# Kernel optimization log

Measured on AMD Instinct MI355X. Metric: run time of the kernel, lower is better.

## Reference

```python
import jax, jax.numpy as jnp
import numpy as np

N = 50000      # nodes
E = 800000     # edges (before self-loops)
D = 128        # input_dim == hidden_dim
L = 3          # num_layers
EPS = 1e-5     # BatchNorm eps


def setup_inputs() -> dict:
    key = jax.random.key(0)
    k0, k1, k2 = jax.random.split(key, 3)
    x = jax.random.normal(k0, (N, D), dtype=jnp.float32)
    edge_index = jax.random.randint(k1, (2, E), 0, N, dtype=jnp.int32)
    # stacked per-layer params (layer 0 is input_dim->hidden, same shape since D==hidden)
    W = jax.random.normal(k2, (L, D, D), dtype=jnp.float32) / np.float32(np.sqrt(D))
    b = jnp.zeros((L, D), dtype=jnp.float32)
    gamma = jnp.ones((L, D), dtype=jnp.float32)
    beta = jnp.zeros((L, D), dtype=jnp.float32)
    return {"x": x, "edge_index": edge_index, "W": W, "b": b, "gamma": gamma, "beta": beta}


def reference(x, edge_index, W, b, gamma, beta):
    # --- GCN symmetric normalization with self-loops (PyG GCNConv default) ---
    loop = jnp.arange(N, dtype=edge_index.dtype)
    src = jnp.concatenate([edge_index[0], loop])      # [E+N]
    dst = jnp.concatenate([edge_index[1], loop])      # [E+N]
    deg = jax.ops.segment_sum(jnp.ones_like(dst, dtype=x.dtype), dst, num_segments=N)
    dinv = jax.lax.rsqrt(deg)                          # deg >= 1 due to self-loops
    norm = (dinv[src] * dinv[dst])[:, None]            # [E+N, 1]

    h = x
    for i in range(L):
        # GCNConv: aggregate norm * (h W)[src] into dst, then bias
        m = h @ W[i]                                   # [N, D]
        h = jax.ops.segment_sum(m[src] * norm, dst, num_segments=N) + b[i]
        # BatchNorm1d (training-mode batch statistics, biased variance)
        mu = jnp.mean(h, axis=0)
        var = jnp.var(h, axis=0)
        h = gamma[i] * (h - mu) * jax.lax.rsqrt(var + EPS) + beta[i]
        # ReLU; dropout is identity in eval mode
        h = jax.nn.relu(h)
    return h
```

## Files before the change

### kernel.cpp

```cpp
#include <hip/hip_runtime.h>
#include <hip/hip_bf16.h>

#define N_NODES 50000
#define N_EDGES 800000
#define DIM 128
#define BN_EPS 1e-5f
#define GATHER_BLOCKS (N_NODES / 4)
#define RED_BLOCKS 125
#define CAP 48

#define PART_SHIFT 7
#define PART_SIZE 128
#define NPARTS ((N_NODES + PART_SIZE - 1) / PART_SIZE)
#define QSTRIDE 32
#define BIN_EPB 4096
#define BIN_BLOCKS ((N_EDGES + BIN_EPB - 1) / BIN_EPB)
#define QCAP2 2560
#define GEMM_BLOCKS (N_NODES / 16)

typedef __attribute__((ext_vector_type(8))) short short8;
typedef __attribute__((ext_vector_type(4))) float float4v;

__device__ __forceinline__ float bf16_bits_to_f32(unsigned short u) {
    union { unsigned int i; float f; } c;
    c.i = ((unsigned int)u) << 16;
    return c.f;
}

__device__ __forceinline__ float bf16_lo(unsigned int u) {
    union { unsigned int i; float f; } c;
    c.i = u << 16;
    return c.f;
}

__device__ __forceinline__ float bf16_hi(unsigned int u) {
    union { unsigned int i; float f; } c;
    c.i = u & 0xFFFF0000u;
    return c.f;
}

__device__ __forceinline__ unsigned short f32_to_bf16_bits(float f) {
    union { float f; unsigned int i; } c;
    c.f = f;
    unsigned int lsb = (c.i >> 16) & 1u;
    c.i += 0x7FFFu + lsb;
    return (unsigned short)(c.i >> 16);
}

__global__ __launch_bounds__(256) void sniff(const unsigned short* __restrict__ xu,
                                             float* __restrict__ mode) {
    __shared__ int cnt;
    if (threadIdx.x == 0) cnt = 0;
    __syncthreads();
    int ok = 0;
    for (int i = threadIdx.x; i < 512; i += 256) {
        unsigned e = (xu[i] >> 7) & 0xFFu;
        if (e >= 96u && e <= 159u) ok++;
    }
    atomicAdd(&cnt, ok);
    __syncthreads();
    if (threadIdx.x == 0) mode[0] = (cnt >= 480) ? 0.0f : 1.0f;
}

__global__ __launch_bounds__(256) void zero_buf(float* __restrict__ p, int n) {
    int i = blockIdx.x * blockDim.x + threadIdx.x;
    if (i < n) p[i] = 0.0f;
}

__global__ __launch_bounds__(256) void zero_int(int* __restrict__ p, int n) {
    int i = blockIdx.x * blockDim.x + threadIdx.x;
    if (i < n) p[i] = 0;
}

__global__ __launch_bounds__(256) void zero_aux(int* __restrict__ qcnt,
                                                float* __restrict__ stats,
                                                int* __restrict__ done) {
    for (int i = threadIdx.x; i < NPARTS; i += 256) qcnt[(size_t)i * QSTRIDE] = 0;
    stats[threadIdx.x] = 0.0f;
    if (threadIdx.x == 0) done[0] = 0;
}

__global__ __launch_bounds__(256) void convert_params(
    const void* __restrict__ W, const void* __restrict__ b,
    const void* __restrict__ g, const void* __restrict__ be,
    const float* __restrict__ mode,
    unsigned short* __restrict__ Wt, float* __restrict__ pf32) {
    const bool mf32 = mode[0] > 0.5f;
    int i = blockIdx.x * blockDim.x + threadIdx.x;
    const int NW = 3 * DIM * DIM;
    if (i < NW) {
        int l = i >> 14;
        int rem = i & 16383;
        int k = rem >> 7;
        int n = rem & 127;
        unsigned short v = mf32 ? f32_to_bf16_bits(((const float*)W)[i])
                                : ((const unsigned short*)W)[i];
        Wt[(size_t)l * DIM * DIM + (size_t)n * DIM + k] = v;
    } else if (i < NW + 3 * 3 * DIM) {
        int p = i - NW;
        int which = p / 384;
        int r = p - which * 384;
        const void* srcp = (which == 0) ? b : (which == 1) ? g : be;
        float v = mf32 ? ((const float*)srcp)[r]
                       : bf16_bits_to_f32(((const unsigned short*)srcp)[r]);
        pf32[which * 384 + r] = v;
    }
}

__global__ __launch_bounds__(256) void fused_a(
    const int* __restrict__ src, const int* __restrict__ dst,
    int* __restrict__ qcnt, unsigned int* __restrict__ queue,
    const void* __restrict__ x, const unsigned short* __restrict__ Wt,
    const float* __restrict__ mode, unsigned short* __restrict__ A) {
    __shared__ int lcnt[NPARTS];
    __shared__ int pref[NPARTS];
    __shared__ int loff[NPARTS];
    __shared__ int gbase[NPARTS];
    __shared__ unsigned int staged2[BIN_EPB];
    __shared__ int sortedN;
    const int bid = blockIdx.x;
    if (bid < BIN_BLOCKS) {
        const int t = threadIdx.x;
        const int blk0 = bid * BIN_EPB;
        const int nval = min(BIN_EPB, N_EDGES - blk0);
        for (int i = t; i < NPARTS; i += 256) lcnt[i] = 0;
        __syncthreads();
        for (int li = t; li < nval; li += 256) {
            int d = dst[blk0 + li];
            if ((unsigned)d < (unsigned)N_NODES)
                atomicAdd(&lcnt[d >> PART_SHIFT], 1);
        }
        __syncthreads();
        if (t < 64) {
            int base = 0;
            for (int c = 0; c < (NPARTS + 63) / 64; ++c) {
                int idx = c * 64 + t;
                int orig = (idx < NPARTS) ? lcnt[idx] : 0;
                int v = orig;
                #pragma unroll
                for (int o = 1; o < 64; o <<= 1) {
                    int up = __shfl_up(v, o);
                    if (t >= o) v += up;
                }
                if (idx < NPARTS) { pref[idx] = base + v - orig; loff[idx] = base + v - orig; }
                base += __shfl(v, 63);
            }
            if (t == 0) sortedN = base;
        }
        __syncthreads();
        for (int i = t; i < NPARTS; i += 256) {
            int c = lcnt[i];
            gbase[i] = c ? atomicAdd(&qcnt[(size_t)i * QSTRIDE], c) : 0;
        }
        __syncthreads();
        for (int li = t; li < nval; li += 256) {
            int d = dst[blk0 + li];
            if ((unsigned)d < (unsigned)N_NODES) {
                int s = src[blk0 + li];
                int part = d >> PART_SHIFT;
                unsigned int pk = (unsigned int)(s & 0xFFFF) |
                                  ((unsigned int)(d & (PART_SIZE - 1)) << 16) |
                                  ((unsigned int)part << 23);
                int pos = atomicAdd(&loff[part], 1);
                staged2[pos] = pk;
            }
        }
        __syncthreads();
        const int nOut = sortedN;
        for (int i = t; i < nOut; i += 256) {
            unsigned int pk = staged2[i];
            int part = pk >> 23;
            int gp = gbase[part] + (i - pref[part]);
            if (gp < QCAP2)
                queue[(size_t)part * QCAP2 + gp] = pk;
        }
        return;
    }
    const int wave = threadIdx.x >> 6;
    const int lane = threadIdx.x & 63;
    const int quad = lane >> 4;
    const int nidx = lane & 15;
    const int row0 = (bid - BIN_BLOCKS) * 16;

    short8 afrag[4];
    if (mode[0] > 0.5f) {
        const float* xf = (const float*)x;
        #pragma unroll
        for (int kk = 0; kk < 4; ++kk) {
            const float4v* xr = (const float4v*)(xf + (size_t)(row0 + nidx) * DIM + kk * 32 + quad * 8);
            float4v p0 = xr[0], p1 = xr[1];
            #pragma unroll
            for (int j = 0; j < 4; ++j) {
                afrag[kk][j]     = (short)f32_to_bf16_bits(p0[j]);
                afrag[kk][4 + j] = (short)f32_to_bf16_bits(p1[j]);
            }
        }
    } else {
        const unsigned short* hu = (const unsigned short*)x;
        #pragma unroll
        for (int kk = 0; kk < 4; ++kk)
            afrag[kk] = *(const short8*)(hu + (size_t)(row0 + nidx) * DIM + kk * 32 + quad * 8);
    }

    short8 bfrag[2][4];
    #pragma unroll
    for (int half = 0; half < 2; ++half) {
        int c = wave * 32 + half * 16 + nidx;
        #pragma unroll
        for (int kk = 0; kk < 4; ++kk)
            bfrag[half][kk] = *(const short8*)(Wt + (size_t)c * DIM + kk * 32 + quad * 8);
    }

    float4v acc0 = {0.f, 0.f, 0.f, 0.f};
    float4v acc1 = {0.f, 0.f, 0.f, 0.f};
    #pragma unroll
    for (int kk = 0; kk < 4; ++kk) {
        acc0 = __builtin_amdgcn_mfma_f32_16x16x32_bf16(afrag[kk], bfrag[0][kk], acc0, 0, 0, 0);
        acc1 = __builtin_amdgcn_mfma_f32_16x16x32_bf16(afrag[kk], bfrag[1][kk], acc1, 0, 0, 0);
    }

    #pragma unroll
    for (int r = 0; r < 4; ++r) {
        int row = row0 + quad * 4 + r;
        size_t i0 = (size_t)row * DIM + wave * 32 + nidx;
        A[i0]      = f32_to_bf16_bits(acc0[r]);
        A[i0 + 16] = f32_to_bf16_bits(acc1[r]);
    }
}

__global__ __launch_bounds__(256) void csr_build(
    const int* __restrict__ qcnt, const unsigned int* __restrict__ queue,
    unsigned short* __restrict__ colu, int* __restrict__ cnt,
    float* __restrict__ dinv) {
    __shared__ int lcnt[PART_SIZE];
    const int p = blockIdx.x;
    if (threadIdx.x < PART_SIZE) lcnt[threadIdx.x] = 0;
    __syncthreads();
    const int base = p << PART_SHIFT;
    const int n = min(qcnt[(size_t)p * QSTRIDE], QCAP2);
    const unsigned int* qp = queue + (size_t)p * QCAP2;
    for (int i = threadIdx.x; i < n; i += 256) {
        unsigned int pk = qp[i];
        int dl = (pk >> 16) & (PART_SIZE - 1);
        int s  = pk & 0xFFFFu;
        int pos = atomicAdd(&lcnt[dl], 1);
        if (pos < CAP)
            colu[(size_t)(base + dl) * CAP + pos] = (unsigned short)s;
    }
    __syncthreads();
    if (threadIdx.x < PART_SIZE) {
        int d = base + threadIdx.x;
        if (d < N_NODES) {
            int c = lcnt[threadIdx.x];
            cnt[d] = c;
            dinv[d] = rsqrtf((float)c + 1.0f);
        }
    }
}

__global__ __launch_bounds__(256) void make_dinv(const int* __restrict__ cnt,
                                                 float* __restrict__ dinv) {
    int v = blockIdx.x * blockDim.x + threadIdx.x;
    if (v < N_NODES) dinv[v] = rsqrtf((float)cnt[v] + 1.0f);
}

__global__ __launch_bounds__(256) void gemm_scale(
    const void* hsrc, int kind, int b_bf16,
    const unsigned short* __restrict__ Wt,
    const float* __restrict__ dinv,
    const float* __restrict__ mode,
    const float* __restrict__ alpha, const float* __restrict__ delta,
    unsigned short* A, float* __restrict__ B, int write_b) {
    const int wave = threadIdx.x >> 6;
    const int lane = threadIdx.x & 63;
    const int quad = lane >> 4;
    const int nidx = lane & 15;
    const int row0 = blockIdx.x * 16;

    short8 afrag[4];
    if (kind == 0) {
        if (mode[0] > 0.5f) {
            const float* xf = (const float*)hsrc;
            #pragma unroll
            for (int kk = 0; kk < 4; ++kk) {
                const float4v* xr = (const float4v*)(xf + (size_t)(row0 + nidx) * DIM + kk * 32 + quad * 8);
                float4v p0 = xr[0], p1 = xr[1];
                #pragma unroll
                for (int j = 0; j < 4; ++j) {
                    afrag[kk][j]     = (short)f32_to_bf16_bits(p0[j]);
                    afrag[kk][4 + j] = (short)f32_to_bf16_bits(p1[j]);
                }
            }
        } else {
            const unsigned short* hu = (const unsigned short*)hsrc;
            #pragma unroll
            for (int kk = 0; kk < 4; ++kk)
                afrag[kk] = *(const short8*)(hu + (size_t)(row0 + nidx) * DIM + kk * 32 + quad * 8);
        }
    } else if (b_bf16) {
        const unsigned short* Bh = (const unsigned short*)hsrc;
        const float dv = dinv[row0 + nidx];
        #pragma unroll
        for (int kk = 0; kk < 4; ++kk) {
            short8 braw = *(const short8*)(Bh + (size_t)(row0 + nidx) * DIM + kk * 32 + quad * 8);
            const float* ap = alpha + kk * 32 + quad * 8;
            const float* dp = delta + kk * 32 + quad * 8;
            float4v A0 = *(const float4v*)ap, A1 = *(const float4v*)(ap + 4);
            float4v D0 = *(const float4v*)dp, D1 = *(const float4v*)(dp + 4);
            #pragma unroll
            for (int j = 0; j < 4; ++j) {
                float v0 = bf16_bits_to_f32((unsigned short)braw[j]);
                float v1 = bf16_bits_to_f32((unsigned short)braw[4 + j]);
                float h0 = fmaxf(fmaf(A0[j] * dv, v0, D0[j]), 0.f);
                float h1 = fmaxf(fmaf(A1[j] * dv, v1, D1[j]), 0.f);
                afrag[kk][j]     = (short)f32_to_bf16_bits(h0);
                afrag[kk][4 + j] = (short)f32_to_bf16_bits(h1);
            }
        }
    } else {
        const float* Bf = (const float*)hsrc;
        const float dv = dinv[row0 + nidx];
        #pragma unroll
        for (int kk = 0; kk < 4; ++kk) {
            const float* bp = Bf + (size_t)(row0 + nidx) * DIM + kk * 32 + quad * 8;
            float4v p0 = *(const float4v*)bp;
            float4v p1 = *(const float4v*)(bp + 4);
            const float* ap = alpha + kk * 32 + quad * 8;
            const float* dp = delta + kk * 32 + quad * 8;
            float4v A0 = *(const float4v*)ap, A1 = *(const float4v*)(ap + 4);
            float4v D0 = *(const float4v*)dp, D1 = *(const float4v*)(dp + 4);
            #pragma unroll
            for (int j = 0; j < 4; ++j) {
                float h0 = fmaxf(fmaf(A0[j] * dv, p0[j], D0[j]), 0.f);
                float h1 = fmaxf(fmaf(A1[j] * dv, p1[j], D1[j]), 0.f);
                afrag[kk][j]     = (short)f32_to_bf16_bits(h0);
                afrag[kk][4 + j] = (short)f32_to_bf16_bits(h1);
            }
        }
    }

    short8 bfrag[2][4];
    #pragma unroll
    for (int half = 0; half < 2; ++half) {
        int c = wave * 32 + half * 16 + nidx;
        #pragma unroll
        for (int kk = 0; kk < 4; ++kk)
            bfrag[half][kk] = *(const short8*)(Wt + (size_t)c * DIM + kk * 32 + quad * 8);
    }

    float4v acc0 = {0.f, 0.f, 0.f, 0.f};
    float4v acc1 = {0.f, 0.f, 0.f, 0.f};
    #pragma unroll
    for (int kk = 0; kk < 4; ++kk) {
        acc0 = __builtin_amdgcn_mfma_f32_16x16x32_bf16(afrag[kk], bfrag[0][kk], acc0, 0, 0, 0);
        acc1 = __builtin_amdgcn_mfma_f32_16x16x32_bf16(afrag[kk], bfrag[1][kk], acc1, 0, 0, 0);
    }

    #pragma unroll
    for (int r = 0; r < 4; ++r) {
        int row = row0 + quad * 4 + r;
        float d = dinv[row];
        float v0 = acc0[r] * d;
        float v1 = acc1[r] * d;
        size_t i0 = (size_t)row * DIM + wave * 32 + nidx;
        size_t i1 = i0 + 16;
        A[i0] = f32_to_bf16_bits(v0);
        A[i1] = f32_to_bf16_bits(v1);
        if (write_b) { B[i0] = v0; B[i1] = v1; }
    }
}

#define ACC4(v, w) do { \
    if (SC) { a0 = fmaf(w, bf16_lo(v.x), a0); a1 = fmaf(w, bf16_hi(v.x), a1); \
              a2 = fmaf(w, bf16_lo(v.y), a2); a3 = fmaf(w, bf16_hi(v.y), a3); } \
    else { a0 += bf16_lo(v.x); a1 += bf16_hi(v.x); \
           a2 += bf16_lo(v.y); a3 += bf16_hi(v.y); } } while (0)

template <int SC>
__global__ __launch_bounds__(256) void gather_csr(
    const int* __restrict__ cnt, const unsigned short* __restrict__ colu,
    const unsigned short* __restrict__ A,
    const float* __restrict__ dinv, const float* __restrict__ bias,
    unsigned short* __restrict__ Bh, float* __restrict__ partial) {
    __shared__ float sacc[4][128], sacc2[4][128];
    const int wave = threadIdx.x >> 6;
    const int lane = threadIdx.x & 63;
    const int half = lane >> 5;
    const int lid  = lane & 31;
    const int cbase = lid * 4;
    const int node = blockIdx.x * 4 + wave;
    const int lo = node * CAP;
    const int hi = lo + min(cnt[node], CAP);
    const float dv = dinv[node];

    float a0 = 0.f, a1 = 0.f, a2 = 0.f, a3 = 0.f;
    if (half == 0) {
        uint2 su = *(const uint2*)(A + (size_t)node * DIM + cbase);
        const float scl = SC ? dv : 1.0f;
        a0 = scl * bf16_lo(su.x); a1 = scl * bf16_hi(su.x);
        a2 = scl * bf16_lo(su.y); a3 = scl * bf16_hi(su.y);
    }

    int e = lo + half;
    for (; e + 14 < hi; e += 16) {
        int s0 = colu[e];      int s1 = colu[e + 2];
        int s2 = colu[e + 4];  int s3 = colu[e + 6];
        int s4 = colu[e + 8];  int s5 = colu[e + 10];
        int s6 = colu[e + 12]; int s7 = colu[e + 14];
        float w0 = SC ? dinv[s0] : 0.f; float w1 = SC ? dinv[s1] : 0.f;
        float w2 = SC ? dinv[s2] : 0.f; float w3 = SC ? dinv[s3] : 0.f;
        float w4 = SC ? dinv[s4] : 0.f; float w5 = SC ? dinv[s5] : 0.f;
        float w6 = SC ? dinv[s6] : 0.f; float w7 = SC ? dinv[s7] : 0.f;
        uint2 v0 = *(const uint2*)(A + (size_t)s0 * DIM + cbase);
        uint2 v1 = *(const uint2*)(A + (size_t)s1 * DIM + cbase);
        uint2 v2 = *(const uint2*)(A + (size_t)s2 * DIM + cbase);
        uint2 v3 = *(const uint2*)(A + (size_t)s3 * DIM + cbase);
        uint2 v4 = *(const uint2*)(A + (size_t)s4 * DIM + cbase);
        uint2 v5 = *(const uint2*)(A + (size_t)s5 * DIM + cbase);
        uint2 v6 = *(const uint2*)(A + (size_t)s6 * DIM + cbase);
        uint2 v7 = *(const uint2*)(A + (size_t)s7 * DIM + cbase);
        ACC4(v0, w0); ACC4(v1, w1); ACC4(v2, w2); ACC4(v3, w3);
        ACC4(v4, w4); ACC4(v5, w5); ACC4(v6, w6); ACC4(v7, w7);
    }
    for (; e + 6 < hi; e += 8) {
        int s0 = colu[e];     int s1 = colu[e + 2];
        int s2 = colu[e + 4]; int s3 = colu[e + 6];
        float w0 = SC ? dinv[s0] : 0.f; float w1 = SC ? dinv[s1] : 0.f;
        float w2 = SC ? dinv[s2] : 0.f; float w3 = SC ? dinv[s3] : 0.f;
        uint2 v0 = *(const uint2*)(A + (size_t)s0 * DIM + cbase);
        uint2 v1 = *(const uint2*)(A + (size_t)s1 * DIM + cbase);
        uint2 v2 = *(const uint2*)(A + (size_t)s2 * DIM + cbase);
        uint2 v3 = *(const uint2*)(A + (size_t)s3 * DIM + cbase);
        ACC4(v0, w0); ACC4(v1, w1); ACC4(v2, w2); ACC4(v3, w3);
    }
    for (; e < hi; e += 2) {
        int s0 = colu[e];
        float w0 = SC ? dinv[s0] : 0.f;
        uint2 v0 = *(const uint2*)(A + (size_t)s0 * DIM + cbase);
        ACC4(v0, w0);
    }

    a0 += __shfl_xor(a0, 32);
    a1 += __shfl_xor(a1, 32);
    a2 += __shfl_xor(a2, 32);
    a3 += __shfl_xor(a3, 32);

    if (half == 0) {
        unsigned int px = (unsigned int)f32_to_bf16_bits(a0) |
                          ((unsigned int)f32_to_bf16_bits(a1) << 16);
        unsigned int py = (unsigned int)f32_to_bf16_bits(a2) |
                          ((unsigned int)f32_to_bf16_bits(a3) << 16);
        uint2 st = {px, py};
        *(uint2*)(Bh + (size_t)node * DIM + cbase) = st;
        float4 bb = *(const float4*)(bias + cbase);
        float v0 = fmaf(dv, a0, bb.x);
        float v1 = fmaf(dv, a1, bb.y);
        float v2 = fmaf(dv, a2, bb.z);
        float v3 = fmaf(dv, a3, bb.w);
        sacc[wave][cbase]     = v0;  sacc2[wave][cbase]     = v0 * v0;
        sacc[wave][cbase + 1] = v1;  sacc2[wave][cbase + 1] = v1 * v1;
        sacc[wave][cbase + 2] = v2;  sacc2[wave][cbase + 2] = v2 * v2;
        sacc[wave][cbase + 3] = v3;  sacc2[wave][cbase + 3] = v3 * v3;
    }
    __syncthreads();
    const int t = threadIdx.x;
    float s;
    if (t < 128) s = sacc[0][t] + sacc[1][t] + sacc[2][t] + sacc[3][t];
    else { int c = t - 128; s = sacc2[0][c] + sacc2[1][c] + sacc2[2][c] + sacc2[3][c]; }
    partial[(size_t)blockIdx.x * 256 + t] = s;
}

__global__ __launch_bounds__(256) void reduce_coefs(
    const float* __restrict__ partial, float* __restrict__ stats,
    int* __restrict__ done, const float* __restrict__ pf32, int l,
    float* __restrict__ alpha, float* __restrict__ delta) {
    const int t = threadIdx.x;
    const int rows = GATHER_BLOCKS / RED_BLOCKS;
    const int r0 = blockIdx.x * rows;
    float s = 0.f;
    for (int i = 0; i < rows; ++i)
        s += partial[(size_t)(r0 + i) * 256 + t];
    atomicAdd(&stats[t], s);
    __threadfence();
    __shared__ int lastFlag;
    if (t == 0) lastFlag = (atomicAdd(done, 1) == RED_BLOCKS - 1) ? 1 : 0;
    __syncthreads();
    if (lastFlag && t < 128) {
        float cs  = atomicAdd(&stats[t], 0.0f);
        float css = atomicAdd(&stats[t + 128], 0.0f);
        const float invN = 1.0f / N_NODES;
        float mu = cs * invN;
        float var = css * invN - mu * mu;
        float istd = rsqrtf(var + BN_EPS);
        float gg = pf32[384 + l * 128 + t];
        float bt = pf32[768 + l * 128 + t];
        float bi = pf32[l * 128 + t];
        float al = gg * istd;
        alpha[t] = al;
        delta[t] = al * (bi - mu) + bt;
        atomicExch(&stats[t], 0.0f);
        atomicExch(&stats[t + 128], 0.0f);
        if (t == 0) atomicExch(done, 0);
    }
}

__global__ __launch_bounds__(128) void bn_coefs(
    const float* __restrict__ pf32, int l,
    float* __restrict__ colsum, float* __restrict__ colsumsq,
    float* __restrict__ alpha, float* __restrict__ delta) {
    int c = threadIdx.x;
    const float invN = 1.0f / N_NODES;
    float mu = colsum[c] * invN;
    float var = colsumsq[c] * invN - mu * mu;
    float istd = rsqrtf(var + BN_EPS);
    float gg = pf32[384 + l * 128 + c];
    float bt = pf32[768 + l * 128 + c];
    float bi = pf32[l * 128 + c];
    float al = gg * istd;
    alpha[c] = al;
    delta[c] = al * (bi - mu) + bt;
    colsum[c] = 0.f;
    colsumsq[c] = 0.f;
}

__global__ __launch_bounds__(256) void hist_dst(const int* __restrict__ dst,
                                                int* __restrict__ cnt) {
    int e = blockIdx.x * blockDim.x + threadIdx.x;
    if (e < N_EDGES) atomicAdd(&cnt[dst[e]], 1);
}

__global__ __launch_bounds__(256) void scatter_edges(
    const int* __restrict__ src, const int* __restrict__ dst,
    const unsigned short* __restrict__ A, float* __restrict__ B) {
    int t = blockIdx.x * blockDim.x + threadIdx.x;
    int e = t >> 4;
    if (e >= N_EDGES) return;
    int f = (t & 15) * 8;
    int s = src[e], d = dst[e];
    short8 v = *(const short8*)(A + (size_t)s * DIM + f);
    float* bp = B + (size_t)d * DIM + f;
    #pragma unroll
    for (int j = 0; j < 8; ++j)
        atomicAdd(bp + j, bf16_bits_to_f32((unsigned short)v[j]));
}

__global__ __launch_bounds__(256) void bn_reduce(
    const float* __restrict__ B, const float* __restrict__ dinv,
    const float* __restrict__ bias,
    float* __restrict__ colsum, float* __restrict__ colsumsq) {
    int c = threadIdx.x & 127;
    int half = threadIdx.x >> 7;
    float bb = bias[c];
    float s = 0.f, s2 = 0.f;
    for (int row = blockIdx.x * 2 + half; row < N_NODES; row += gridDim.x * 2) {
        float v = dinv[row] * B[(size_t)row * DIM + c] + bb;
        s += v;
        s2 += v * v;
    }
    __shared__ float ls[128], ls2[128];
    if (half == 1) { ls[c] = s; ls2[c] = s2; }
    __syncthreads();
    if (half == 0) {
        atomicAdd(&colsum[c], s + ls[c]);
        atomicAdd(&colsumsq[c], s2 + ls2[c]);
    }
}

__global__ __launch_bounds__(256) void bn_apply(
    const void* __restrict__ Bv, int b_bf16,
    const float* __restrict__ dinv,
    const float* __restrict__ alpha, const float* __restrict__ delta,
    const float* __restrict__ mode, void* __restrict__ out) {
    int t = blockIdx.x * blockDim.x + threadIdx.x;
    if (t >= N_NODES * DIM) return;
    int row = t >> 7, c = t & 127;
    float bval = b_bf16 ? bf16_bits_to_f32(((const unsigned short*)Bv)[t])
                        : ((const float*)Bv)[t];
    float r = fmaxf(fmaf(alpha[c] * dinv[row], bval, delta[c]), 0.f);
    if (mode[0] > 0.5f)
        ((float*)out)[t] = r;
    else
        ((unsigned short*)out)[t] = f32_to_bf16_bits(r);
}

extern "C" void kernel_launch(void* const* d_in, const int* in_sizes, int n_in,
                              void* d_out, int out_size, void* d_ws, size_t ws_size,
                              hipStream_t stream) {
    const void* x  = d_in[0];
    const int*  ei = (const int*)d_in[1];
    const void* W  = d_in[2];
    const void* b  = d_in[3];
    const void* g  = d_in[4];
    const void* be = d_in[5];

    unsigned short* hA = (unsigned short*)d_out;

    char* ws = (char*)d_ws;
    size_t off = 0;
    auto alloc = [&](size_t bytes) {
        char* p = ws + off;
        off = (off + bytes + 255) & ~(size_t)255;
        return p;
    };
    float* dinv     = (float*)alloc((size_t)N_NODES * 4);
    float* B        = (float*)alloc((size_t)N_NODES * DIM * 4);
    unsigned short* Wt = (unsigned short*)alloc((size_t)3 * DIM * DIM * 2);
    float* pf32     = (float*)alloc(3 * 3 * DIM * 4);
    float* stats    = (float*)alloc(256 * 4);
    float* alphaB   = (float*)alloc(128 * 4);
    float* deltaB   = (float*)alloc(128 * 4);
    float* mode     = (float*)alloc(64 * 4);
    int*   done     = (int*)alloc(64 * 4);
    int*   cnt      = (int*)alloc((size_t)N_NODES * 4);
    unsigned short* colu = (unsigned short*)alloc((size_t)N_NODES * CAP * 2);
    float* partial  = (float*)alloc((size_t)GATHER_BLOCKS * 256 * 4);
    int*   qcnt     = (int*)alloc((size_t)NPARTS * QSTRIDE * 4);
    unsigned int* queue = (unsigned int*)partial;
    const bool csr_ok = (ws_size >= off) || (ws_size == 0);
    float* colsum = stats;
    float* colsumsq = stats + 128;
    unsigned short* Bh = (unsigned short*)B;

    const int* srcv = ei;
    const int* dstv = ei + N_EDGES;

    sniff<<<1, 256, 0, stream>>>((const unsigned short*)x, mode);
    convert_params<<<(3 * DIM * DIM + 3 * 3 * DIM + 255) / 256, 256, 0, stream>>>(
        W, b, g, be, mode, Wt, pf32);

    if (csr_ok) {
        zero_aux<<<1, 256, 0, stream>>>(qcnt, stats, done);
        fused_a<<<BIN_BLOCKS + GEMM_BLOCKS, 256, 0, stream>>>(
            srcv, dstv, qcnt, queue, x, Wt, mode, hA);
        csr_build<<<NPARTS, 256, 0, stream>>>(qcnt, queue, colu, cnt, dinv);

        for (int l = 0; l < 3; ++l) {
            if (l > 0)
                gemm_scale<<<GEMM_BLOCKS, 256, 0, stream>>>(
                    (const void*)B, 2, 1, Wt + (size_t)l * DIM * DIM, dinv, mode,
                    alphaB, deltaB, hA, B, 0);
            if (l == 0)
                gather_csr<1><<<GATHER_BLOCKS, 256, 0, stream>>>(
                    cnt, colu, hA, dinv, pf32 + l * 128, Bh, partial);
            else
                gather_csr<0><<<GATHER_BLOCKS, 256, 0, stream>>>(
                    cnt, colu, hA, dinv, pf32 + l * 128, Bh, partial);
            reduce_coefs<<<RED_BLOCKS, 256, 0, stream>>>(
                partial, stats, done, pf32, l, alphaB, deltaB);
            if (l == 2)
                bn_apply<<<(N_NODES * DIM) / 256, 256, 0, stream>>>(
                    (const void*)B, 1, dinv, alphaB, deltaB, mode, d_out);
        }
    } else {
        zero_int<<<(N_NODES + 255) / 256, 256, 0, stream>>>(cnt, N_NODES);
        zero_buf<<<1, 256, 0, stream>>>(stats, 256);
        hist_dst<<<(N_EDGES + 255) / 256, 256, 0, stream>>>(dstv, cnt);
        make_dinv<<<(N_NODES + 255) / 256, 256, 0, stream>>>(cnt, dinv);

        for (int l = 0; l < 3; ++l) {
            const void* hin = (l == 0) ? x : (const void*)B;
            gemm_scale<<<GEMM_BLOCKS, 256, 0, stream>>>(
                hin, (l == 0) ? 0 : 2, 0, Wt + (size_t)l * DIM * DIM, dinv, mode,
                alphaB, deltaB, hA, B, 1);
            scatter_edges<<<(N_EDGES * 16) / 256, 256, 0, stream>>>(srcv, dstv, hA, B);
            bn_reduce<<<256, 256, 0, stream>>>(B, dinv, pf32 + l * 128, colsum, colsumsq);
            bn_coefs<<<1, 128, 0, stream>>>(pf32, l, colsum, colsumsq, alphaB, deltaB);
            if (l == 2)
                bn_apply<<<(N_NODES * DIM) / 256, 256, 0, stream>>>(
                    (const void*)B, 0, dinv, alphaB, deltaB, mode, d_out);
        }
    }
}
```

Measured before the change: 351.8 us.

## Stage edge indices as 16-bit in binning and widen gather to 16-byte loads

```diff
diff --git a/kernel.cpp b/kernel.cpp
--- a/kernel.cpp
+++ b/kernel.cpp
@@ -113,10 +113,9 @@
     const void* __restrict__ x, const unsigned short* __restrict__ Wt,
     const float* __restrict__ mode, unsigned short* __restrict__ A) {
     __shared__ int lcnt[NPARTS];
-    __shared__ int pref[NPARTS];
     __shared__ int loff[NPARTS];
-    __shared__ int gbase[NPARTS];
-    __shared__ unsigned int staged2[BIN_EPB];
+    __shared__ int adj[NPARTS];
+    __shared__ unsigned short staged16[BIN_EPB];
     __shared__ int sortedN;
     const int bid = blockIdx.x;
     if (bid < BIN_BLOCKS) {
@@ -142,7 +141,7 @@
                     int up = __shfl_up(v, o);
                     if (t >= o) v += up;
                 }
-                if (idx < NPARTS) { pref[idx] = base + v - orig; loff[idx] = base + v - orig; }
+                if (idx < NPARTS) loff[idx] = base + v - orig;
                 base += __shfl(v, 63);
             }
             if (t == 0) sortedN = base;
@@ -150,29 +149,30 @@
         __syncthreads();
         for (int i = t; i < NPARTS; i += 256) {
             int c = lcnt[i];
-            gbase[i] = c ? atomicAdd(&qcnt[(size_t)i * QSTRIDE], c) : 0;
+            int gb = c ? atomicAdd(&qcnt[(size_t)i * QSTRIDE], c) : 0;
+            adj[i] = gb - loff[i];
         }
         __syncthreads();
         for (int li = t; li < nval; li += 256) {
             int d = dst[blk0 + li];
             if ((unsigned)d < (unsigned)N_NODES) {
-                int s = src[blk0 + li];
                 int part = d >> PART_SHIFT;
-                unsigned int pk = (unsigned int)(s & 0xFFFF) |
-                                  ((unsigned int)(d & (PART_SIZE - 1)) << 16) |
-                                  ((unsigned int)part << 23);
                 int pos = atomicAdd(&loff[part], 1);
-                staged2[pos] = pk;
+                staged16[pos] = (unsigned short)li;
             }
         }
         __syncthreads();
         const int nOut = sortedN;
         for (int i = t; i < nOut; i += 256) {
-            unsigned int pk = staged2[i];
-            int part = pk >> 23;
-            int gp = gbase[part] + (i - pref[part]);
-            if (gp < QCAP2)
-                queue[(size_t)part * QCAP2 + gp] = pk;
+            int li = staged16[i];
+            int d = dst[blk0 + li];
+            int s = src[blk0 + li];
+            int part = d >> PART_SHIFT;
+            int gp = adj[part] + i;
+            if (gp >= 0 && gp < QCAP2)
+                queue[(size_t)part * QCAP2 + gp] =
+                    (unsigned int)(s & 0xFFFF) |
+                    ((unsigned int)(d & (PART_SIZE - 1)) << 16);
         }
         return;
     }
@@ -370,11 +370,11 @@
     }
 }
 
-#define ACC4(v, w) do { \
-    if (SC) { a0 = fmaf(w, bf16_lo(v.x), a0); a1 = fmaf(w, bf16_hi(v.x), a1); \
-              a2 = fmaf(w, bf16_lo(v.y), a2); a3 = fmaf(w, bf16_hi(v.y), a3); } \
-    else { a0 += bf16_lo(v.x); a1 += bf16_hi(v.x); \
-           a2 += bf16_lo(v.y); a3 += bf16_hi(v.y); } } while (0)
+#define FMA8(vv, ww) do { \
+    a0 = fmaf(ww, bf16_lo(vv.x), a0); a1 = fmaf(ww, bf16_hi(vv.x), a1); \
+    a2 = fmaf(ww, bf16_lo(vv.y), a2); a3 = fmaf(ww, bf16_hi(vv.y), a3); \
+    a4 = fmaf(ww, bf16_lo(vv.z), a4); a5 = fmaf(ww, bf16_hi(vv.z), a5); \
+    a6 = fmaf(ww, bf16_lo(vv.w), a6); a7 = fmaf(ww, bf16_hi(vv.w), a7); } while (0)
 
 template <int SC>
 __global__ __launch_bounds__(256) void gather_csr(
@@ -385,82 +385,68 @@
     __shared__ float sacc[4][128], sacc2[4][128];
     const int wave = threadIdx.x >> 6;
     const int lane = threadIdx.x & 63;
-    const int half = lane >> 5;
-    const int lid  = lane & 31;
-    const int cbase = lid * 4;
+    const int g    = lane >> 4;
+    const int c8   = (lane & 15) * 8;
     const int node = blockIdx.x * 4 + wave;
-    const int lo = node * CAP;
-    const int hi = lo + min(cnt[node], CAP);
+    const int deg  = min(cnt[node], CAP);
+    const int lo   = node * CAP;
     const float dv = dinv[node];
 
-    float a0 = 0.f, a1 = 0.f, a2 = 0.f, a3 = 0.f;
-    if (half == 0) {
-        uint2 su = *(const uint2*)(A + (size_t)node * DIM + cbase);
-        const float scl = SC ? dv : 1.0f;
-        a0 = scl * bf16_lo(su.x); a1 = scl * bf16_hi(su.x);
-        a2 = scl * bf16_lo(su.y); a3 = scl * bf16_hi(su.y);
-    }
-
-    int e = lo + half;
-    for (; e + 14 < hi; e += 16) {
-        int s0 = colu[e];      int s1 = colu[e + 2];
-        int s2 = colu[e + 4];  int s3 = colu[e + 6];
-        int s4 = colu[e + 8];  int s5 = colu[e + 10];
-        int s6 = colu[e + 12]; int s7 = colu[e + 14];
-        float w0 = SC ? dinv[s0] : 0.f; float w1 = SC ? dinv[s1] : 0.f;
-        float w2 = SC ? dinv[s2] : 0.f; float w3 = SC ? dinv[s3] : 0.f;
-        float w4 = SC ? dinv[s4] : 0.f; float w5 = SC ? dinv[s5] : 0.f;
-        float w6 = SC ? dinv[s6] : 0.f; float w7 = SC ? dinv[s7] : 0.f;
-        uint2 v0 = *(const uint2*)(A + (size_t)s0 * DIM + cbase);
-        uint2 v1 = *(const uint2*)(A + (size_t)s1 * DIM + cbase);
-        uint2 v2 = *(const uint2*)(A + (size_t)s2 * DIM + cbase);
-        uint2 v3 = *(const uint2*)(A + (size_t)s3 * DIM + cbase);
-        uint2 v4 = *(const uint2*)(A + (size_t)s4 * DIM + cbase);
-        uint2 v5 = *(const uint2*)(A + (size_t)s5 * DIM + cbase);
-        uint2 v6 = *(const uint2*)(A + (size_t)s6 * DIM + cbase);
-        uint2 v7 = *(const uint2*)(A + (size_t)s7 * DIM + cbase);
-        ACC4(v0, w0); ACC4(v1, w1); ACC4(v2, w2); ACC4(v3, w3);
-        ACC4(v4, w4); ACC4(v5, w5); ACC4(v6, w6); ACC4(v7, w7);
-    }
-    for (; e + 6 < hi; e += 8) {
-        int s0 = colu[e];     int s1 = colu[e + 2];
-        int s2 = colu[e + 4]; int s3 = colu[e + 6];
-        float w0 = SC ? dinv[s0] : 0.f; float w1 = SC ? dinv[s1] : 0.f;
-        float w2 = SC ? dinv[s2] : 0.f; float w3 = SC ? dinv[s3] : 0.f;
-        uint2 v0 = *(const uint2*)(A + (size_t)s0 * DIM + cbase);
-        uint2 v1 = *(const uint2*)(A + (size_t)s1 * DIM + cbase);
-        uint2 v2 = *(const uint2*)(A + (size_t)s2 * DIM + cbase);
-        uint2 v3 = *(const uint2*)(A + (size_t)s3 * DIM + cbase);
-        ACC4(v0, w0); ACC4(v1, w1); ACC4(v2, w2); ACC4(v3, w3);
-    }
-    for (; e < hi; e += 2) {
-        int s0 = colu[e];
-        float w0 = SC ? dinv[s0] : 0.f;
-        uint2 v0 = *(const uint2*)(A + (size_t)s0 * DIM + cbase);
-        ACC4(v0, w0);
-    }
-
-    a0 += __shfl_xor(a0, 32);
-    a1 += __shfl_xor(a1, 32);
-    a2 += __shfl_xor(a2, 32);
-    a3 += __shfl_xor(a3, 32);
-
-    if (half == 0) {
-        unsigned int px = (unsigned int)f32_to_bf16_bits(a0) |
-                          ((unsigned int)f32_to_bf16_bits(a1) << 16);
-        unsigned int py = (unsigned int)f32_to_bf16_bits(a2) |
-                          ((unsigned int)f32_to_bf16_bits(a3) << 16);
-        uint2 st = {px, py};
-        *(uint2*)(Bh + (size_t)node * DIM + cbase) = st;
-        float4 bb = *(const float4*)(bias + cbase);
-        float v0 = fmaf(dv, a0, bb.x);
-        float v1 = fmaf(dv, a1, bb.y);
-        float v2 = fmaf(dv, a2, bb.z);
-        float v3 = fmaf(dv, a3, bb.w);
-        sacc[wave][cbase]     = v0;  sacc2[wave][cbase]     = v0 * v0;
-        sacc[wave][cbase + 1] = v1;  sacc2[wave][cbase + 1] = v1 * v1;
-        sacc[wave][cbase + 2] = v2;  sacc2[wave][cbase + 2] = v2 * v2;
-        sacc[wave][cbase + 3] = v3;  sacc2[wave][cbase + 3] = v3 * v3;
+    int   cv = (lane < deg) ? (int)colu[lo + lane] : 0;
+    float wv = (lane < deg) ? (SC ? dinv[cv] : 1.0f) : 0.0f;
+
+    float a0, a1, a2, a3, a4, a5, a6, a7;
+    {
+        uint4 sv = *(const uint4*)(A + (size_t)node * DIM + c8);
+        const float scl = (g == 0) ? (SC ? dv : 1.0f) : 0.0f;
+        a0 = scl * bf16_lo(sv.x); a1 = scl * bf16_hi(sv.x);
+        a2 = scl * bf16_lo(sv.y); a3 = scl * bf16_hi(sv.y);
+        a4 = scl * bf16_lo(sv.z); a5 = scl * bf16_hi(sv.z);
+        a6 = scl * bf16_lo(sv.w); a7 = scl * bf16_hi(sv.w);
+    }
+
+    const int rounds = (deg + 7) >> 3;
+    int j = 0;
+    for (int r = 0; r < rounds; ++r, j += 8) {
+        int   iA = j + g,  iB = j + 4 + g;
+        int   sA = __shfl(cv, iA);  float wA = __shfl(wv, iA);
+        int   sB = __shfl(cv, iB);  float wB = __shfl(wv, iB);
+        uint4 vA = *(const uint4*)(A + (size_t)sA * DIM + c8);
+        uint4 vB = *(const uint4*)(A + (size_t)sB * DIM + c8);
+        FMA8(vA, wA);
+        FMA8(vB, wB);
+    }
+
+    a0 += __shfl_xor(a0, 16); a0 += __shfl_xor(a0, 32);
+    a1 += __shfl_xor(a1, 16); a1 += __shfl_xor(a1, 32);
+    a2 += __shfl_xor(a2, 16); a2 += __shfl_xor(a2, 32);
+    a3 += __shfl_xor(a3, 16); a3 += __shfl_xor(a3, 32);
+    a4 += __shfl_xor(a4, 16); a4 += __shfl_xor(a4, 32);
+    a5 += __shfl_xor(a5, 16); a5 += __shfl_xor(a5, 32);
+    a6 += __shfl_xor(a6, 16); a6 += __shfl_xor(a6, 32);
+    a7 += __shfl_xor(a7, 16); a7 += __shfl_xor(a7, 32);
+
+    if (lane < 16) {
+        unsigned int p0 = (unsigned int)f32_to_bf16_bits(a0) | ((unsigned int)f32_to_bf16_bits(a1) << 16);
+        unsigned int p1 = (unsigned int)f32_to_bf16_bits(a2) | ((unsigned int)f32_to_bf16_bits(a3) << 16);
+        unsigned int p2 = (unsigned int)f32_to_bf16_bits(a4) | ((unsigned int)f32_to_bf16_bits(a5) << 16);
+        unsigned int p3 = (unsigned int)f32_to_bf16_bits(a6) | ((unsigned int)f32_to_bf16_bits(a7) << 16);
+        uint4 st = {p0, p1, p2, p3};
+        *(uint4*)(Bh + (size_t)node * DIM + c8) = st;
+        float4 b0 = *(const float4*)(bias + c8);
+        float4 b1 = *(const float4*)(bias + c8 + 4);
+        float v0 = fmaf(dv, a0, b0.x), v1 = fmaf(dv, a1, b0.y);
+        float v2 = fmaf(dv, a2, b0.z), v3 = fmaf(dv, a3, b0.w);
+        float v4 = fmaf(dv, a4, b1.x), v5 = fmaf(dv, a5, b1.y);
+        float v6 = fmaf(dv, a6, b1.z), v7 = fmaf(dv, a7, b1.w);
+        sacc[wave][c8]     = v0;  sacc2[wave][c8]     = v0 * v0;
+        sacc[wave][c8 + 1] = v1;  sacc2[wave][c8 + 1] = v1 * v1;
+        sacc[wave][c8 + 2] = v2;  sacc2[wave][c8 + 2] = v2 * v2;
+        sacc[wave][c8 + 3] = v3;  sacc2[wave][c8 + 3] = v3 * v3;
+        sacc[wave][c8 + 4] = v4;  sacc2[wave][c8 + 4] = v4 * v4;
+        sacc[wave][c8 + 5] = v5;  sacc2[wave][c8 + 5] = v5 * v5;
+        sacc[wave][c8 + 6] = v6;  sacc2[wave][c8 + 6] = v6 * v6;
+        sacc[wave][c8 + 7] = v7;  sacc2[wave][c8 + 7] = v7 * v7;
     }
     __syncthreads();
     const int t = threadIdx.x;
```

New measurement: 338.9 us. 1.04x faster.
